# Optimization experiments

Measured on AMD Instinct MI355X. Metric: run time of the kernel, lower is better.

Reference implementation:

```python
import jax, jax.numpy as jnp
import numpy as np


def chamfer_l2(x, y):
    # x: [B,N1,3], y: [B,N2,3]; squared-L2 pairwise distances via Gram trick
    x2 = jnp.sum(x * x, axis=-1)                     # [B,N1]
    y2 = jnp.sum(y * y, axis=-1)                     # [B,N2]
    xy = jnp.einsum('bnd,bmd->bnm', x, y)            # [B,N1,N2]
    d = x2[:, :, None] + y2[:, None, :] - 2.0 * xy   # [B,N1,N2]
    cham_x = jnp.min(d, axis=2)                      # [B,N1] min over gt
    cham_y = jnp.min(d, axis=1)                      # [B,N2] min over pred
    return jnp.mean(cham_x) + jnp.mean(cham_y)


def setup_inputs() -> dict:
    key = jax.random.key(0)
    k1, k2, k3 = jax.random.split(key, 3)
    B = 4
    coarse_pc = jax.random.normal(k1, (B, 1024, 3), dtype=jnp.float32)
    fine_pc = jax.random.normal(k2, (B, 8192, 3), dtype=jnp.float32)
    gt_pc = jax.random.normal(k3, (B, 8192, 3), dtype=jnp.float32)
    return {"coarse_pc": coarse_pc, "fine_pc": fine_pc, "gt_pc": gt_pc,
            "param_coarse": 1000, "param_fine": 1000}


def reference(coarse_pc, fine_pc, gt_pc, param_coarse, param_fine):
    loss_coarse = chamfer_l2(coarse_pc, gt_pc) * param_coarse
    loss_fine = chamfer_l2(fine_pc, gt_pc) * param_fine
    return jnp.stack([loss_coarse, loss_fine])
```

## Files before the change

kernel.cpp:

```cpp
#include <hip/hip_runtime.h>

constexpr int NMINS = 102400;
constexpr int NBLK  = 2304;

typedef __attribute__((ext_vector_type(8)))  short bf16x8;
typedef __attribute__((ext_vector_type(16))) float f32x16;

__device__ __forceinline__ void split2(float v, unsigned& h, unsigned& l) {
    const unsigned uh = __float_as_uint(v) & 0xFFFF0000u;
    h = uh >> 16;
    l = __float_as_uint(v - __uint_as_float(uh)) >> 16;
}


__global__ __launch_bounds__(256, 4) void pccl_stage(
    const float* __restrict__ Xc, const float* __restrict__ Xf,
    const float* __restrict__ G, unsigned* __restrict__ mins)
{
    __shared__ uint4 alo[512];
    __shared__ uint4 ahi[512];
    const int tid  = threadIdx.x;
    const int lane = tid & 63;
    const int l31  = lane & 31;
    const bool hi  = lane >= 32;
    const int wv   = __builtin_amdgcn_readfirstlane(tid >> 6);
    const int W    = blockIdx.x;

    const float* Xp; const float* Yp;
    int NX, NY, ls, lc, local, mbase;
    if (W < 128)        { Xp=Xc; Yp=G;  NX=1024; NY=8192; ls=4; lc=1; local=W;      mbase=0; }
    else if (W < 256)   { Xp=G;  Yp=Xc; NX=8192; NY=1024; ls=1; lc=4; local=W-128;  mbase=4096; }
    else if (W < 1280)  { Xp=Xf; Yp=G;  NX=8192; NY=8192; ls=4; lc=4; local=W-256;  mbase=36864; }
    else                { Xp=G;  Yp=Xf; NX=8192; NY=8192; ls=4; lc=4; local=W-1280; mbase=69632; }
    const int split  = local & ((1 << ls) - 1);
    const int rest   = local >> ls;
    const int chunk4 = rest & ((1 << lc) - 1);
    const int b      = rest >> lc;

    const float* yg = Yp + ((size_t)b * NY + (size_t)split * 512) * 3;
    #pragma unroll
    for (int it = 0; it < 2; ++it) {
        const int pt = tid + 256 * it;
        const float y0 = yg[pt*3+0], y1 = yg[pt*3+1], y2 = yg[pt*3+2];
        const float w  = fmaf(y0, y0, fmaf(y1, y1, y2 * y2));
        unsigned h0, L0, h1, L1, h2, L2, hw, Lw;
        split2(y0, h0, L0); split2(y1, h1, L1);
        split2(y2, h2, L2); split2(w,  hw, Lw);
        alo[pt] = make_uint4(h0 | (L0 << 16), h0 | (h1 << 16),
                             L1 | (h1 << 16), h2 | (L2 << 16));
        ahi[pt] = make_uint4(h2 | (hw << 16), Lw, 0u, 0u);
    }

    const float* xg = Xp + ((size_t)b * NX + (size_t)chunk4 * 512 + (size_t)wv * 128) * 3;
    bf16x8 Bf[4]; float x2s[4];
    #pragma unroll
    for (int f = 0; f < 4; ++f) {
        const int p = f * 32 + l31;
        const float x0 = xg[p*3+0], x1 = xg[p*3+1], x2 = xg[p*3+2];
        x2s[f] = fmaf(x0, x0, fmaf(x1, x1, x2 * x2));
        unsigned sh0, sl0, sh1, sl1, sh2, sl2;
        split2(-2.f * x0, sh0, sl0);
        split2(-2.f * x1, sh1, sl1);
        split2(-2.f * x2, sh2, sl2);
        union { unsigned u[4]; bf16x8 v; } bu;
        bu.u[0] = hi ? (sl2 | (0x3F80u << 16)) : (sh0 | (sh0 << 16));
        bu.u[1] = hi ? 0x3F80u                 : (sl0 | (sh1 << 16));
        bu.u[2] = hi ? 0u                      : (sh1 | (sl1 << 16));
        bu.u[3] = hi ? 0u                      : (sh2 | (sh2 << 16));
        Bf[f] = bu.v;
    }

    float best[4][4];
    #pragma unroll
    for (int f = 0; f < 4; ++f)
        #pragma unroll
        for (int j = 0; j < 4; ++j) best[f][j] = 3.0e38f;

    const f32x16 zc = (f32x16)0.0f;
    const uint4* __restrict__ abase = hi ? ahi : alo;

    __syncthreads();

    #define FOLD(f, acc)                                                      \
        {                                                                     \
            _Pragma("unroll")                                                 \
            for (int j = 0; j < 4; ++j) {                                     \
                const float t3 = fminf(fminf((acc)[4*j], (acc)[4*j+1]),       \
                                       (acc)[4*j+2]);                         \
                best[f][j] = fminf(fminf(best[f][j], t3), (acc)[4*j+3]);      \
            }                                                                 \
        }

    #pragma unroll 2
    for (int t = 0; t < 16; ++t) {
        const uint4 dd = abase[t * 32 + l31];
        union { uint4 u; bf16x8 v; } au; au.u = dd;
        const bf16x8 Af = au.v;
        #pragma unroll
        for (int fp = 0; fp < 2; ++fp) {
            const int f0 = fp * 2, f1 = fp * 2 + 1;
            const f32x16 a0 = __builtin_amdgcn_mfma_f32_32x32x16_bf16(Af, Bf[f0], zc, 0, 0, 0);
            const f32x16 a1 = __builtin_amdgcn_mfma_f32_32x32x16_bf16(Af, Bf[f1], zc, 0, 0, 0);
            FOLD(f0, a0);
            FOLD(f1, a1);
        }
    }
    #undef FOLD

    unsigned* mp = mins + mbase + b * NX + chunk4 * 512 + wv * 128;
    #pragma unroll
    for (int f = 0; f < 4; ++f) {
        float tm = fminf(fminf(best[f][0], best[f][1]),
                         fminf(best[f][2], best[f][3]));
        tm = fminf(tm, __shfl_xor(tm, 32, 64));
        const float d = fmaxf(x2s[f] + tm, 0.0f);
        atomicMin(mp + f * 32 + l31, __float_as_uint(d));
    }
}

__global__ __launch_bounds__(1024) void pccl_sum(
    const unsigned* __restrict__ mins,
    const int* __restrict__ pc, const int* __restrict__ pf,
    float* __restrict__ out)
{
    const int tid = threadIdx.x;
    const int lane = tid & 63;
    const int wv = tid >> 6;
    float w0 = 0.f, w1 = 0.f;
    #pragma unroll 5
    for (int k = 0; k < 25; ++k) {
        const int q = tid + 1024 * k;
        const uint4 v = ((const uint4*)mins)[q];
        const float s = __uint_as_float(v.x) + __uint_as_float(v.y)
                      + __uint_as_float(v.z) + __uint_as_float(v.w);
        if (q < 1024)       w0 += s * (1.f / 4096.f);
        else if (q < 9216)  w0 += s * (1.f / 32768.f);
        else                w1 += s * (1.f / 32768.f);
    }
    #pragma unroll
    for (int off = 1; off < 64; off <<= 1) {
        w0 += __shfl_xor(w0, off, 64);
        w1 += __shfl_xor(w1, off, 64);
    }
    __shared__ float s0[16], s1[16];
    if (lane == 0) { s0[wv] = w0; s1[wv] = w1; }
    __syncthreads();
    if (tid == 0) {
        float a0 = 0.f, a1 = 0.f;
        #pragma unroll
        for (int i = 0; i < 16; ++i) { a0 += s0[i]; a1 += s1[i]; }
        out[0] = a0 * (float)pc[0];
        out[1] = a1 * (float)pf[0];
    }
}

extern "C" void kernel_launch(void* const* d_in, const int* in_sizes, int n_in,
                              void* d_out, int out_size, void* d_ws, size_t ws_size,
                              hipStream_t stream) {
    const float* coarse = (const float*)d_in[0];
    const float* fine   = (const float*)d_in[1];
    const float* gt     = (const float*)d_in[2];
    const int*   pc     = (const int*)d_in[3];
    const int*   pf     = (const int*)d_in[4];
    float* out = (float*)d_out;
    unsigned* mins = (unsigned*)d_ws;

    pccl_stage<<<NBLK, 256, 0, stream>>>(coarse, fine, gt, mins);
    pccl_sum<<<1, 1024, 0, stream>>>(mins, pc, pf, out);
}
```

Before: 85.32 us.

## Replace global atomicMin with per-split partial minima and parallel reduction

Each block now writes its partial per-point minimum to a dedicated slot indexed by its y-split instead of issuing atomicMin into a shared array. A multi-block sum kernel then takes the min across splits and accumulates the scaled means into the output with atomicAdd after a memset. This removes atomic contention and the uninitialised-min dependency and spreads the final reduction over 100 blocks. In exchange it uses a much larger workspace, reads more partials, and adds a memset launch.

```diff
diff --git a/kernel.cpp b/kernel.cpp
--- a/kernel.cpp
+++ b/kernel.cpp
@@ -1,7 +1,6 @@
 #include <hip/hip_runtime.h>
 
-constexpr int NMINS = 102400;
-constexpr int NBLK  = 2304;
+constexpr int NBLK = 2304;
 
 typedef __attribute__((ext_vector_type(8)))  short bf16x8;
 typedef __attribute__((ext_vector_type(16))) float f32x16;
@@ -15,7 +14,7 @@
 
 __global__ __launch_bounds__(256, 4) void pccl_stage(
     const float* __restrict__ Xc, const float* __restrict__ Xf,
-    const float* __restrict__ G, unsigned* __restrict__ mins)
+    const float* __restrict__ G, float* __restrict__ mins2)
 {
     __shared__ uint4 alo[512];
     __shared__ uint4 ahi[512];
@@ -29,9 +28,9 @@
     const float* Xp; const float* Yp;
     int NX, NY, ls, lc, local, mbase;
     if (W < 128)        { Xp=Xc; Yp=G;  NX=1024; NY=8192; ls=4; lc=1; local=W;      mbase=0; }
-    else if (W < 256)   { Xp=G;  Yp=Xc; NX=8192; NY=1024; ls=1; lc=4; local=W-128;  mbase=4096; }
-    else if (W < 1280)  { Xp=Xf; Yp=G;  NX=8192; NY=8192; ls=4; lc=4; local=W-256;  mbase=36864; }
-    else                { Xp=G;  Yp=Xf; NX=8192; NY=8192; ls=4; lc=4; local=W-1280; mbase=69632; }
+    else if (W < 256)   { Xp=G;  Yp=Xc; NX=8192; NY=1024; ls=1; lc=4; local=W-128;  mbase=65536; }
+    else if (W < 1280)  { Xp=Xf; Yp=G;  NX=8192; NY=8192; ls=4; lc=4; local=W-256;  mbase=131072; }
+    else                { Xp=G;  Yp=Xf; NX=8192; NY=8192; ls=4; lc=4; local=W-1280; mbase=655360; }
     const int split  = local & ((1 << ls) - 1);
     const int rest   = local >> ls;
     const int chunk4 = rest & ((1 << lc) - 1);
@@ -107,36 +106,40 @@
     }
     #undef FOLD
 
-    unsigned* mp = mins + mbase + b * NX + chunk4 * 512 + wv * 128;
+    const int NXtot = NX * 4;
+    float* mp = mins2 + mbase + (size_t)split * NXtot
+              + b * NX + chunk4 * 512 + wv * 128;
     #pragma unroll
     for (int f = 0; f < 4; ++f) {
         float tm = fminf(fminf(best[f][0], best[f][1]),
                          fminf(best[f][2], best[f][3]));
         tm = fminf(tm, __shfl_xor(tm, 32, 64));
-        const float d = fmaxf(x2s[f] + tm, 0.0f);
-        atomicMin(mp + f * 32 + l31, __float_as_uint(d));
+        mp[f * 32 + l31] = fmaxf(x2s[f] + tm, 0.0f);
     }
 }
 
 __global__ __launch_bounds__(1024) void pccl_sum(
-    const unsigned* __restrict__ mins,
+    const float* __restrict__ mins2,
     const int* __restrict__ pc, const int* __restrict__ pf,
     float* __restrict__ out)
 {
-    const int tid = threadIdx.x;
+    const int tid  = threadIdx.x;
     const int lane = tid & 63;
-    const int wv = tid >> 6;
-    float w0 = 0.f, w1 = 0.f;
-    #pragma unroll 5
-    for (int k = 0; k < 25; ++k) {
-        const int q = tid + 1024 * k;
-        const uint4 v = ((const uint4*)mins)[q];
-        const float s = __uint_as_float(v.x) + __uint_as_float(v.y)
-                      + __uint_as_float(v.z) + __uint_as_float(v.w);
-        if (q < 1024)       w0 += s * (1.f / 4096.f);
-        else if (q < 9216)  w0 += s * (1.f / 32768.f);
-        else                w1 += s * (1.f / 32768.f);
-    }
+    const int wv   = tid >> 6;
+    const int gid  = blockIdx.x * 1024 + tid;
+
+    int base, nsp, x, NXtot; float scale; int o;
+    if (gid < 4096)       { base = 0;      nsp = 16; x = gid;         NXtot = 4096;  scale = 1.f/4096.f;  o = 0; }
+    else if (gid < 36864) { base = 65536;  nsp = 2;  x = gid - 4096;  NXtot = 32768; scale = 1.f/32768.f; o = 0; }
+    else if (gid < 69632) { base = 131072; nsp = 16; x = gid - 36864; NXtot = 32768; scale = 1.f/32768.f; o = 1; }
+    else                  { base = 655360; nsp = 16; x = gid - 69632; NXtot = 32768; scale = 1.f/32768.f; o = 1; }
+
+    float m = mins2[base + x];
+    for (int s = 1; s < nsp; ++s)
+        m = fminf(m, mins2[base + s * NXtot + x]);
+    const float v = m * scale;
+    float w0 = (o == 0) ? v : 0.f;
+    float w1 = (o == 1) ? v : 0.f;
     #pragma unroll
     for (int off = 1; off < 64; off <<= 1) {
         w0 += __shfl_xor(w0, off, 64);
@@ -149,8 +152,8 @@
         float a0 = 0.f, a1 = 0.f;
         #pragma unroll
         for (int i = 0; i < 16; ++i) { a0 += s0[i]; a1 += s1[i]; }
-        out[0] = a0 * (float)pc[0];
-        out[1] = a1 * (float)pf[0];
+        if (a0 != 0.f) atomicAdd(out + 0, a0 * (float)pc[0]);
+        if (a1 != 0.f) atomicAdd(out + 1, a1 * (float)pf[0]);
     }
 }
 
@@ -163,8 +166,9 @@
     const int*   pc     = (const int*)d_in[3];
     const int*   pf     = (const int*)d_in[4];
     float* out = (float*)d_out;
-    unsigned* mins = (unsigned*)d_ws;
+    float* mins2 = (float*)d_ws;
 
-    pccl_stage<<<NBLK, 256, 0, stream>>>(coarse, fine, gt, mins);
-    pccl_sum<<<1, 1024, 0, stream>>>(mins, pc, pf, out);
+    hipMemsetAsync(out, 0, 2 * sizeof(float), stream);
+    pccl_stage<<<NBLK, 256, 0, stream>>>(coarse, fine, gt, mins2);
+    pccl_sum<<<100, 1024, 0, stream>>>(mins2, pc, pf, out);
 }
```

New measurement: 87.67 us. 2.8% more time.
